# Kernel tuning notes

Hardware: AMD Instinct MI355X
Metric: run time of the kernel (lower is better)

## Reference

```python
import jax, jax.numpy as jnp
import numpy as np

B, T, I, H = 256, 512, 64, 256  # batch, seq_len, NUM_BANDS, HIDDEN_DIM; NUM_LAYERS=2


def setup_inputs() -> dict:
    key = jax.random.key(0)
    ks = jax.random.split(key, 12)
    s = 0.05
    f = jnp.float32
    return {
        "x": jax.random.normal(ks[0], (B, T, I), f),
        # layer 0 (input -> hidden)
        "W_ih0": jax.random.normal(ks[1], (H, I), f) * s,
        "W_hh0": jax.random.normal(ks[2], (H, H), f) * s,
        "b_ih0": jax.random.normal(ks[3], (H,), f) * s,
        "b_hh0": jax.random.normal(ks[4], (H,), f) * s,
        # layer 1 (hidden -> hidden)
        "W_ih1": jax.random.normal(ks[5], (H, H), f) * s,
        "W_hh1": jax.random.normal(ks[6], (H, H), f) * s,
        "b_ih1": jax.random.normal(ks[7], (H,), f) * s,
        "b_hh1": jax.random.normal(ks[8], (H,), f) * s,
        # fc head (hidden -> 1)
        "W_fc": jax.random.normal(ks[9], (1, H), f) * s,
        "b_fc": jax.random.normal(ks[10], (1,), f) * s,
    }


def _rnn_layer(x_seq, W_ih, W_hh, b_ih, b_hh):
    """Elman ReLU layer: h_t = relu(W_ih x_t + b_ih + W_hh h_{t-1} + b_hh).
    x_seq: [B, T, D] -> returns [B, T, H]. Input projection is batched; only
    the hidden recurrence runs in the scan."""
    pre = jnp.einsum('btd,hd->bth', x_seq, W_ih) + b_ih + b_hh  # [B,T,H]
    h0 = jnp.zeros((x_seq.shape[0], W_hh.shape[0]), x_seq.dtype)

    def step(h, p_t):
        h = jax.nn.relu(p_t + h @ W_hh.T)
        return h, h

    _, ys = jax.lax.scan(step, h0, jnp.swapaxes(pre, 0, 1))  # [T,B,H]
    return jnp.swapaxes(ys, 0, 1)


def reference(x, W_ih0, W_hh0, b_ih0, b_hh0, W_ih1, W_hh1, b_ih1, b_hh1, W_fc, b_fc):
    h1 = _rnn_layer(x, W_ih0, W_hh0, b_ih0, b_hh0)
    h2 = _rnn_layer(h1, W_ih1, W_hh1, b_ih1, b_hh1)
    out = h2.reshape(-1, h2.shape[-1]) @ W_fc.T + b_fc  # [B*T, 1]
    return out.reshape(-1)
```

## Files before the change

kernel.cpp:

```cpp
#include <hip/hip_runtime.h>


#define T_ 512
#define H_ 256

typedef __attribute__((ext_vector_type(8))) short short8;
typedef __attribute__((ext_vector_type(4))) float f32x4;

#define MFMA(a, b, c) __builtin_amdgcn_mfma_f32_16x16x32_bf16(a, b, c, 0, 0, 0)

__device__ __forceinline__ unsigned short bf16rne(float f) {
    unsigned u = __float_as_uint(f);
    u += 0x7fff + ((u >> 16) & 1);
    return (unsigned short)(u >> 16);
}

__device__ __forceinline__ void split8(const float4 a0, const float4 a1,
                                       short8& hi, short8& lo) {
    const float v[8] = {a0.x, a0.y, a0.z, a0.w, a1.x, a1.y, a1.z, a1.w};
#pragma unroll
    for (int j = 0; j < 8; ++j) {
        unsigned short hb = bf16rne(v[j]);
        float hf = __uint_as_float(((unsigned)hb) << 16);
        unsigned short lb = bf16rne(v[j] - hf);
        hi[j] = (short)hb;
        lo[j] = (short)lb;
    }
}

__global__ __launch_bounds__(256) void k_gemm0(
    const float* __restrict__ x, const float* __restrict__ Wih,
    const float* __restrict__ bih, const float* __restrict__ bhh,
    float* __restrict__ buf)
{
    const int tid = threadIdx.x, lane = tid & 63, wv = tid >> 6;
    const int l15 = lane & 15, lg = lane >> 4;
    const int bc = blockIdx.x & 15;
    const int t0 = (blockIdx.x >> 4) * 32;

    short8 bhi[4][2], blo[4][2];
    f32x4 bias[4];
#pragma unroll
    for (int nt = 0; nt < 4; ++nt) {
        const int n = wv * 64 + nt * 16 + l15;
#pragma unroll
        for (int ks = 0; ks < 2; ++ks) {
            const float4* p = (const float4*)(Wih + (size_t)n * 64 + ks * 32 + 8 * lg);
            split8(p[0], p[1], bhi[nt][ks], blo[nt][ks]);
        }
        const float b = bih[n] + bhh[n];
        bias[nt] = f32x4{b, b, b, b};
    }
#pragma unroll 1
    for (int t = t0; t < t0 + 32; ++t) {
        short8 ahi[2], alo[2];
#pragma unroll
        for (int ks = 0; ks < 2; ++ks) {
            const float4* p =
                (const float4*)(x + ((size_t)(bc * 16 + l15) * T_ + t) * 64 + ks * 32 + 8 * lg);
            split8(p[0], p[1], ahi[ks], alo[ks]);
        }
        f32x4 acc[4];
#pragma unroll
        for (int nt = 0; nt < 4; ++nt) acc[nt] = bias[nt];
#pragma unroll
        for (int ks = 0; ks < 2; ++ks) {
#pragma unroll
            for (int nt = 0; nt < 4; ++nt) acc[nt] = MFMA(ahi[ks], bhi[nt][ks], acc[nt]);
#pragma unroll
            for (int nt = 0; nt < 4; ++nt) acc[nt] = MFMA(alo[ks], bhi[nt][ks], acc[nt]);
#pragma unroll
            for (int nt = 0; nt < 4; ++nt) acc[nt] = MFMA(ahi[ks], blo[nt][ks], acc[nt]);
        }
        float* slot = buf + ((size_t)bc * T_ + t) * 4096;
#pragma unroll
        for (int nt = 0; nt < 4; ++nt)
            *(f32x4*)(slot + (wv * 64 + nt * 16 + l15) * 16 + 4 * lg) = acc[nt];
    }
}

__global__ __launch_bounds__(256, 1) void k_gemm1(
    const float* __restrict__ Wih, const float* __restrict__ bih,
    const float* __restrict__ bhh, float* __restrict__ buf)
{
    const int tid = threadIdx.x, lane = tid & 63, wv = tid >> 6;
    const int l15 = lane & 15, lg = lane >> 4;
    const int bc = blockIdx.x & 15;
    const int t0 = (blockIdx.x >> 4) * 32;

    short8 bhi[4][8], blo[4][8];
    f32x4 bias[4];
#pragma unroll
    for (int nt = 0; nt < 4; ++nt) {
        const int n = wv * 64 + nt * 16 + l15;
#pragma unroll
        for (int ks = 0; ks < 8; ++ks) {
            const float4* p = (const float4*)(Wih + (size_t)n * H_ + ks * 32 + 8 * lg);
            split8(p[0], p[1], bhi[nt][ks], blo[nt][ks]);
        }
        const float b = bih[n] + bhh[n];
        bias[nt] = f32x4{b, b, b, b};
    }
#pragma unroll 1
    for (int t = t0; t < t0 + 32; ++t) {
        float* slot = buf + ((size_t)bc * T_ + t) * 4096;
        const unsigned short* g = (const unsigned short*)slot;
        short8 ahi[8];
#pragma unroll
        for (int ks = 0; ks < 8; ++ks)
            ahi[ks] = *(const short8*)(g + (size_t)l15 * H_ + ks * 32 + 8 * lg);
        __syncthreads();
        f32x4 acc[4];
#pragma unroll
        for (int nt = 0; nt < 4; ++nt) acc[nt] = bias[nt];
#pragma unroll
        for (int ks = 0; ks < 8; ++ks) {
#pragma unroll
            for (int nt = 0; nt < 4; ++nt) acc[nt] = MFMA(ahi[ks], bhi[nt][ks], acc[nt]);
#pragma unroll
            for (int nt = 0; nt < 4; ++nt) acc[nt] = MFMA(ahi[ks], blo[nt][ks], acc[nt]);
        }
#pragma unroll
        for (int nt = 0; nt < 4; ++nt)
            *(f32x4*)(slot + (wv * 64 + nt * 16 + l15) * 16 + 4 * lg) = acc[nt];
    }
}

template <bool WRITE_H1, bool FC>
__global__ __launch_bounds__(512, 1) void k_rnn(
    float* __restrict__ buf, const float* __restrict__ Whh,
    const float* __restrict__ Wfc, const float* __restrict__ bfcp,
    float* __restrict__ out)
{
    const int tid = threadIdx.x, lane = tid & 63, wv = tid >> 6;
    const int l15 = lane & 15, lg = lane >> 4;
    const int bc = blockIdx.x;

    short8 bhi[2][8], blo[2][8];
#pragma unroll
    for (int nt = 0; nt < 2; ++nt) {
        const int n = wv * 32 + nt * 16 + l15;
#pragma unroll
        for (int ks = 0; ks < 8; ++ks) {
            const float4* p = (const float4*)(Whh + (size_t)n * H_ + ks * 32 + 8 * lg);
            split8(p[0], p[1], bhi[nt][ks], blo[nt][ks]);
        }
    }
    float wfc2[2];
    float bfc = 0.f;
    if (FC) {
#pragma unroll
        for (int nt = 0; nt < 2; ++nt) wfc2[nt] = Wfc[wv * 32 + nt * 16 + l15];
        bfc = bfcp[0];
    }

    __shared__ unsigned short hb[2][16][264];
    __shared__ float wavesum[2][8][16];

    for (int i = tid; i < (int)(sizeof(hb) / 16); i += 512)
        ((uint4*)hb)[i] = make_uint4(0u, 0u, 0u, 0u);
    __syncthreads();

    float* slot0 = buf + (size_t)bc * T_ * 4096;
    f32x4 cfrag[2];
#pragma unroll
    for (int nt = 0; nt < 2; ++nt)
        cfrag[nt] = *(const f32x4*)(slot0 + (wv * 32 + nt * 16 + l15) * 16 + 4 * lg);

    int p = 0;
#pragma unroll 1
    for (int t = 0; t < T_; ++t) {
        f32x4 cnext[2];
        if (t + 1 < T_) {
#pragma unroll
            for (int nt = 0; nt < 2; ++nt)
                cnext[nt] = *(const f32x4*)(slot0 + (size_t)(t + 1) * 4096 +
                                            (wv * 32 + nt * 16 + l15) * 16 + 4 * lg);
        }
        short8 ahi[8];
#pragma unroll
        for (int ks = 0; ks < 8; ++ks)
            ahi[ks] = *(const short8*)&hb[p][l15][ks * 32 + 8 * lg];
        f32x4 acc[2];
#pragma unroll
        for (int nt = 0; nt < 2; ++nt) acc[nt] = cfrag[nt];
#pragma unroll
        for (int ks = 0; ks < 8; ++ks) {
#pragma unroll
            for (int nt = 0; nt < 2; ++nt) acc[nt] = MFMA(ahi[ks], bhi[nt][ks], acc[nt]);
#pragma unroll
            for (int nt = 0; nt < 2; ++nt) acc[nt] = MFMA(ahi[ks], blo[nt][ks], acc[nt]);
        }
        float fcp[4] = {0.f, 0.f, 0.f, 0.f};
#pragma unroll
        for (int nt = 0; nt < 2; ++nt) {
            const int n = wv * 32 + nt * 16 + l15;
#pragma unroll
            for (int j = 0; j < 4; ++j) {
                float v = fmaxf(acc[nt][j], 0.f);
                hb[p ^ 1][4 * lg + j][n] = bf16rne(v);
                if (FC) fcp[j] = fmaf(v, wfc2[nt], fcp[j]);
            }
        }
        if (FC) {
#pragma unroll
            for (int j = 0; j < 4; ++j) {
                float f = fcp[j];
                f += __shfl_xor(f, 1, 64);
                f += __shfl_xor(f, 2, 64);
                f += __shfl_xor(f, 4, 64);
                f += __shfl_xor(f, 8, 64);
                fcp[j] = f;
            }
            if (l15 == 0) {
#pragma unroll
                for (int j = 0; j < 4; ++j) wavesum[p][wv][4 * lg + j] = fcp[j];
            }
        }
        __syncthreads();
        if (WRITE_H1) {
            unsigned short* g = (unsigned short*)(slot0 + (size_t)t * 4096);
            const int rr = tid >> 5, c = (tid & 31) * 8;
            *(uint4*)(g + rr * H_ + c) = *(const uint4*)&hb[p ^ 1][rr][c];
        }
        if (FC) {
            if (wv == 0 && lane < 16) {
                float s = bfc;
#pragma unroll
                for (int w8 = 0; w8 < 8; ++w8) s += wavesum[p][w8][lane];
                out[(size_t)(bc * 16 + lane) * T_ + t] = s;
            }
        }
#pragma unroll
        for (int nt = 0; nt < 2; ++nt) cfrag[nt] = cnext[nt];
        p ^= 1;
    }
}

extern "C" void kernel_launch(void* const* d_in, const int* in_sizes, int n_in,
                              void* d_out, int out_size, void* d_ws, size_t ws_size,
                              hipStream_t stream) {
    (void)in_sizes; (void)n_in; (void)out_size; (void)ws_size;
    const float* x    = (const float*)d_in[0];
    const float* Wih0 = (const float*)d_in[1];
    const float* Whh0 = (const float*)d_in[2];
    const float* bih0 = (const float*)d_in[3];
    const float* bhh0 = (const float*)d_in[4];
    const float* Wih1 = (const float*)d_in[5];
    const float* Whh1 = (const float*)d_in[6];
    const float* bih1 = (const float*)d_in[7];
    const float* bhh1 = (const float*)d_in[8];
    const float* Wfc  = (const float*)d_in[9];
    const float* bfc  = (const float*)d_in[10];

    float* buf = (float*)d_ws;
    float* out = (float*)d_out;

    k_gemm0<<<dim3(256), dim3(256), 0, stream>>>(x, Wih0, bih0, bhh0, buf);
    k_rnn<true, false><<<dim3(16), dim3(512), 0, stream>>>(buf, Whh0, Wfc, bfc, out);
    k_gemm1<<<dim3(256), dim3(256), 0, stream>>>(Wih1, bih1, bhh1, buf);
    k_rnn<false, true><<<dim3(16), dim3(512), 0, stream>>>(buf, Whh1, Wfc, bfc, out);
}
```

Baseline: 1.414 ms.

## Use fragment-native LDS layout for hidden state and split MFMA accumulators

Stores the bf16 hidden state in LDS and in the global h1 buffer in an MFMA-fragment-ordered layout, so the per-step A-operand loads are contiguous and the padded 2D array is no longer needed. The layer-0 GEMM read path is changed to match. The hi and lo weight products now go into separate accumulators, which shortens each serial MFMA dependency chain in the latency-bound recurrence. __syncthreads is replaced with an explicit lgkmcnt wait plus s_barrier. An odd empty loop and zero-initialised cnext are also added; they add clutter but do not change the work done.

```diff
diff --git a/kernel.cpp b/kernel.cpp
--- a/kernel.cpp
+++ b/kernel.cpp
@@ -26,6 +26,14 @@
         hi[j] = (short)hb;
         lo[j] = (short)lb;
     }
+}
+
+__device__ __forceinline__ void lds_sync() {
+    asm volatile("s_waitcnt lgkmcnt(0)" ::: "memory");
+    __builtin_amdgcn_sched_barrier(0);
+    __builtin_amdgcn_s_barrier();
+    __builtin_amdgcn_sched_barrier(0);
+    asm volatile("" ::: "memory");
 }
 
 __global__ __launch_bounds__(256) void k_gemm0(
@@ -108,7 +116,7 @@
         short8 ahi[8];
 #pragma unroll
         for (int ks = 0; ks < 8; ++ks)
-            ahi[ks] = *(const short8*)(g + (size_t)l15 * H_ + ks * 32 + 8 * lg);
+            ahi[ks] = *(const short8*)(g + ks * 512 + lg * 128 + l15 * 8);
         __syncthreads();
         f32x4 acc[4];
 #pragma unroll
@@ -154,9 +162,11 @@
         bfc = bfcp[0];
     }
 
-    __shared__ unsigned short hb[2][16][264];
+    __shared__ unsigned short hb[2][4096];
     __shared__ float wavesum[2][8][16];
 
+    for (int i = tid; i < 512; ++i == 0 ? i : i)
+        ;
     for (int i = tid; i < (int)(sizeof(hb) / 16); i += 512)
         ((uint4*)hb)[i] = make_uint4(0u, 0u, 0u, 0u);
     __syncthreads();
@@ -170,7 +180,7 @@
     int p = 0;
 #pragma unroll 1
     for (int t = 0; t < T_; ++t) {
-        f32x4 cnext[2];
+        f32x4 cnext[2] = {f32x4{0.f, 0.f, 0.f, 0.f}, f32x4{0.f, 0.f, 0.f, 0.f}};
         if (t + 1 < T_) {
 #pragma unroll
             for (int nt = 0; nt < 2; ++nt)
@@ -180,25 +190,28 @@
         short8 ahi[8];
 #pragma unroll
         for (int ks = 0; ks < 8; ++ks)
-            ahi[ks] = *(const short8*)&hb[p][l15][ks * 32 + 8 * lg];
-        f32x4 acc[2];
-#pragma unroll
-        for (int nt = 0; nt < 2; ++nt) acc[nt] = cfrag[nt];
-#pragma unroll
-        for (int ks = 0; ks < 8; ++ks) {
-#pragma unroll
-            for (int nt = 0; nt < 2; ++nt) acc[nt] = MFMA(ahi[ks], bhi[nt][ks], acc[nt]);
-#pragma unroll
-            for (int nt = 0; nt < 2; ++nt) acc[nt] = MFMA(ahi[ks], blo[nt][ks], acc[nt]);
+            ahi[ks] = *(const short8*)&hb[p][ks * 512 + lg * 128 + l15 * 8];
+        f32x4 accA[2], accB[2];
+#pragma unroll
+        for (int nt = 0; nt < 2; ++nt) {
+            accA[nt] = cfrag[nt];
+            accB[nt] = f32x4{0.f, 0.f, 0.f, 0.f};
+        }
+#pragma unroll
+        for (int ks = 0; ks < 8; ++ks) {
+#pragma unroll
+            for (int nt = 0; nt < 2; ++nt) accA[nt] = MFMA(ahi[ks], bhi[nt][ks], accA[nt]);
+#pragma unroll
+            for (int nt = 0; nt < 2; ++nt) accB[nt] = MFMA(ahi[ks], blo[nt][ks], accB[nt]);
         }
         float fcp[4] = {0.f, 0.f, 0.f, 0.f};
 #pragma unroll
         for (int nt = 0; nt < 2; ++nt) {
-            const int n = wv * 32 + nt * 16 + l15;
+            const int gbase = (wv * 4 + nt * 2 + (l15 >> 3)) * 128 + (l15 & 7);
 #pragma unroll
             for (int j = 0; j < 4; ++j) {
-                float v = fmaxf(acc[nt][j], 0.f);
-                hb[p ^ 1][4 * lg + j][n] = bf16rne(v);
+                float v = fmaxf(accA[nt][j] + accB[nt][j], 0.f);
+                hb[p ^ 1][gbase + (4 * lg + j) * 8] = bf16rne(v);
                 if (FC) fcp[j] = fmaf(v, wfc2[nt], fcp[j]);
             }
         }
@@ -217,11 +230,10 @@
                 for (int j = 0; j < 4; ++j) wavesum[p][wv][4 * lg + j] = fcp[j];
             }
         }
-        __syncthreads();
+        lds_sync();
         if (WRITE_H1) {
-            unsigned short* g = (unsigned short*)(slot0 + (size_t)t * 4096);
-            const int rr = tid >> 5, c = (tid & 31) * 8;
-            *(uint4*)(g + rr * H_ + c) = *(const uint4*)&hb[p ^ 1][rr][c];
+            unsigned short* gst = (unsigned short*)(slot0 + (size_t)t * 4096);
+            *(uint4*)(gst + tid * 8) = *(const uint4*)&hb[p ^ 1][tid * 8];
         }
         if (FC) {
             if (wv == 0 && lane < 16) {
```

Result: no change. 1.410 ms (-0.3%).
